# Kernel optimization log

Hardware: AMD Instinct MI355X
Metric: run time of the kernel (lower is better)

## Reference

```python
import jax, jax.numpy as jnp
import numpy as np

L = 5        # n_layers
H = 1024     # dim_in (hidden size)
DOUT = 1     # dim_out (input_size of LSTM)
T = 128      # curve_resolution
BS = 512


def setup_inputs() -> dict:
    key = jax.random.key(0)
    ks = jax.random.split(key, 8)
    s = 1.0 / np.sqrt(H)  # PyTorch LSTM default init scale U(-1/sqrt(H), 1/sqrt(H))
    x = jax.random.normal(ks[0], (BS, H), jnp.float32)
    W_ih0 = jax.random.normal(ks[1], (4 * H, DOUT), jnp.float32) * s
    W_ih_rest = jax.random.normal(ks[2], (L - 1, 4 * H, H), jnp.float32) * s
    W_hh = jax.random.normal(ks[3], (L, 4 * H, H), jnp.float32) * s
    b_ih = jax.random.normal(ks[4], (L, 4 * H), jnp.float32) * s
    b_hh = jax.random.normal(ks[5], (L, 4 * H), jnp.float32) * s
    W_ro = jax.random.normal(ks[6], (DOUT, H), jnp.float32) * s
    b_ro = jax.random.normal(ks[7], (DOUT,), jnp.float32) * s
    return {"x": x, "W_ih0": W_ih0, "W_ih_rest": W_ih_rest, "W_hh": W_hh,
            "b_ih": b_ih, "b_hh": b_hh, "W_ro": W_ro, "b_ro": b_ro}


def _cell(xin, h, c, W_ih, W_hh_l, b_ih_l, b_hh_l):
    # PyTorch gate order: i, f, g, o
    gates = xin @ W_ih.T + h @ W_hh_l.T + (b_ih_l + b_hh_l)
    i, f, g, o = jnp.split(gates, 4, axis=-1)
    c_new = jax.nn.sigmoid(f) * c + jax.nn.sigmoid(i) * jnp.tanh(g)
    h_new = jax.nn.sigmoid(o) * jnp.tanh(c_new)
    return h_new, c_new


def reference(x, W_ih0, W_ih_rest, W_hh, b_ih, b_hh, W_ro, b_ro):
    bs = x.shape[0]
    h0 = jnp.tile(x[None], (L, 1, 1))  # (L, bs, H) — graph emb as both h and c
    c0 = h0
    inp0 = jnp.zeros((bs, DOUT), x.dtype)

    def step(carry, _):
        h, c, inp = carry
        hs, cs = [], []
        xin = inp
        for l in range(L):
            W_ih_l = W_ih0 if l == 0 else W_ih_rest[l - 1]
            h_l, c_l = _cell(xin, h[l], c[l], W_ih_l, W_hh[l], b_ih[l], b_hh[l])
            hs.append(h_l)
            cs.append(c_l)
            xin = h_l
        out = xin @ W_ro.T + b_ro  # readout, fed back as next input
        return (jnp.stack(hs), jnp.stack(cs), out), out

    _, ys = jax.lax.scan(step, (h0, c0, inp0), None, length=T)
    return jnp.transpose(ys, (1, 0, 2))  # (bs, T, DOUT)
```

## Files before the change

kernel.cpp:

```cpp
#include <hip/hip_runtime.h>
#include <hip/hip_fp16.h>

#define LL 5
#define H 1024
#define G 4096
#define T 128
#define BS 512
#define BSH (BS * H)
#define BSG (BS * G)
#define GH  (G * H)

typedef _Float16 f16x8 __attribute__((ext_vector_type(8)));
typedef float f32x4 __attribute__((ext_vector_type(4)));

__device__ __forceinline__ float sigmoidf_(float x) { return 1.f / (1.f + __expf(-x)); }
__device__ __forceinline__ float tanhf_(float x) { return 2.f / (1.f + __expf(-2.f * x)) - 1.f; }

__device__ __forceinline__ void gll16(const void* g, void* l) {
  __builtin_amdgcn_global_load_lds(
      (const __attribute__((address_space(1))) void*)g,
      (__attribute__((address_space(3))) void*)l, 16, 0, 0);
}

#define VMW(N) asm volatile("s_waitcnt vmcnt(" #N ")" ::: "memory")
#define SBAR() asm volatile("s_barrier" ::: "memory")


__global__ void k_convert(const float* __restrict__ Whf, const float* __restrict__ Wxf,
                          __half* __restrict__ Whb, __half* __restrict__ Wxb) {
  const long long n1 = (long long)LL * GH / 4;
  const long long n2 = (long long)(LL - 1) * GH / 4;
  long long i = (long long)blockIdx.x * blockDim.x + threadIdx.x;
  long long stride = (long long)gridDim.x * blockDim.x;
  for (long long v = i; v < n1 + n2; v += stride) {
    const float4* src; __half* dst; long long idx;
    if (v < n1) { src = (const float4*)Whf; dst = Whb; idx = v; }
    else        { src = (const float4*)Wxf; dst = Wxb; idx = v - n1; }
    float4 f = src[idx];
    ushort4 u;
    u.x = __half_as_ushort(__float2half(f.x));
    u.y = __half_as_ushort(__float2half(f.y));
    u.z = __half_as_ushort(__float2half(f.z));
    u.w = __half_as_ushort(__float2half(f.w));
    ((ushort4*)dst)[idx] = u;
  }
}

__global__ void k_bias_y(const float* __restrict__ bih, const float* __restrict__ bhh,
                         float* __restrict__ bias, float* __restrict__ y0,
                         float* __restrict__ y1) {
  int i = blockIdx.x * blockDim.x + threadIdx.x;
  if (i < LL * G) bias[i] = bih[i] + bhh[i];
  if (i < BS) { y0[i] = 0.f; y1[i] = 0.f; }
}

__global__ void k_init(const float* __restrict__ x, __half* __restrict__ hbuf,
                       float* __restrict__ c) {
  int i = blockIdx.x * blockDim.x + threadIdx.x;
  if (i >= BS * H) return;
  float v = x[i];
  __half hb = __float2half(v);
  for (int l = 0; l < LL; l++) {
    hbuf[(long long)l * BSH + i] = hb;
    c[(long long)l * BSH + i] = v;
  }
}


#define SH_HALFS 24576

__device__ __forceinline__ void stage_tile(const __half* __restrict__ A,
                                           const __half* __restrict__ W,
                                           int m0, int jb, int kb,
                                           __half* aB, __half* bB,
                                           int wave, int lane) {
  const int i8 = lane >> 3;
  const int j8 = lane & 7;
  const int kch = j8 ^ i8;
#pragma unroll
  for (int s = 0; s < 2; s++) {
    int c = wave * 2 + s;
    int row = c * 8 + i8;
    gll16(A + (m0 + row) * H + kb + kch * 8, aB + c * 512);
  }
#pragma unroll
  for (int s = 0; s < 4; s++) {
    int c = wave * 4 + s;
    int row = c * 8 + i8;
    int grow = (row >> 5) * H + jb + (row & 31);
    gll16(W + grow * H + kb + kch * 8, bB + c * 512);
  }
}

__device__ __forceinline__ void compute_tile(const __half* aB, const __half* bB,
                                             int wave, int lane, f32x4 acc[2][4]) {
  const int quad = lane >> 4, col = lane & 15;
  const int wm = wave >> 1, wn = wave & 1;
  const int sw = col & 7;
#pragma unroll
  for (int ks = 0; ks < 2; ks++) {
    const int kc = ks * 4 + quad;
    const int kcs = kc ^ sw;
    f16x8 af[2], bf[4];
#pragma unroll
    for (int mt = 0; mt < 2; mt++) {
      int r = wm * 32 + mt * 16 + col;
      af[mt] = *(const f16x8*)(aB + ((r << 3) + kcs) * 8);
    }
#pragma unroll
    for (int nt = 0; nt < 4; nt++) {
      int n = nt * 32 + wn * 16 + col;
      bf[nt] = *(const f16x8*)(bB + ((n << 3) + kcs) * 8);
    }
#pragma unroll
    for (int mt = 0; mt < 2; mt++)
#pragma unroll
      for (int nt = 0; nt < 4; nt++)
        acc[mt][nt] = __builtin_amdgcn_mfma_f32_16x16x32_f16(af[mt], bf[nt], acc[mt][nt], 0, 0, 0);
  }
}

__device__ __forceinline__ void gemm_async(const __half* __restrict__ A,
                                           const __half* __restrict__ W,
                                           int m0, int jb, __half* sh, int t,
                                           f32x4 acc[2][4]) {
  const int wave = t >> 6, lane = t & 63;
  stage_tile(A, W, m0, jb, 0, sh, sh + 4096, wave, lane);
  for (int it = 0; it < 15; ++it) {
    const int cur = it & 1;
    stage_tile(A, W, m0, jb, (it + 1) * 64,
               sh + (cur ? 0 : 12288), sh + (cur ? 4096 : 16384), wave, lane);
    VMW(6);
    SBAR();
    compute_tile(sh + (cur ? 12288 : 0), sh + (cur ? 16384 : 4096), wave, lane, acc);
    SBAR();
  }
  VMW(0);
  SBAR();
  compute_tile(sh + 12288, sh + 16384, wave, lane, acc);
}

__device__ __forceinline__ void epilogue_store(f32x4 acc[2][4], __half* __restrict__ Ghout,
                                               const float* __restrict__ biasS,
                                               int m0, int jb, int t) {
  const int lane = t & 63, wave = t >> 6;
  const int quad = lane >> 4, col = lane & 15;
  const int wm = wave >> 1, wn = wave & 1;
  const int j = jb + wn * 16 + col;
  float bs[4];
#pragma unroll
  for (int nt = 0; nt < 4; nt++) bs[nt] = biasS[nt * H + j];
#pragma unroll
  for (int mt = 0; mt < 2; mt++)
#pragma unroll
    for (int nt = 0; nt < 4; nt++)
#pragma unroll
      for (int r = 0; r < 4; r++) {
        int b = m0 + wm * 32 + mt * 16 + quad * 4 + r;
        Ghout[b * G + nt * H + j] = __float2half(acc[mt][nt][r] + bs[nt]);
      }
}

__device__ __forceinline__ void epilogue_cell(f32x4 acc[2][4],
                                              const __half* __restrict__ Ghin,
                                              float* __restrict__ c, __half* __restrict__ hout,
                                              int m0, int jb, int t,
                                              const float* __restrict__ Wro,
                                              float* __restrict__ yAcc, float* red) {
  const int lane = t & 63, wave = t >> 6;
  const int quad = lane >> 4, col = lane & 15;
  const int wm = wave >> 1, wn = wave & 1;
  const int j = jb + wn * 16 + col;
  const float wj = Wro ? Wro[j] : 0.f;
#pragma unroll
  for (int mt = 0; mt < 2; mt++)
#pragma unroll
    for (int r = 0; r < 4; r++) {
      int row = wm * 32 + mt * 16 + quad * 4 + r;
      int b = m0 + row;
      float gi = acc[mt][0][r] + __half2float(Ghin[b * G + j]);
      float gf = acc[mt][1][r] + __half2float(Ghin[b * G + H + j]);
      float gg = acc[mt][2][r] + __half2float(Ghin[b * G + 2 * H + j]);
      float go = acc[mt][3][r] + __half2float(Ghin[b * G + 3 * H + j]);
      float cold = c[b * H + j];
      float cn = sigmoidf_(gf) * cold + sigmoidf_(gi) * tanhf_(gg);
      float hn = sigmoidf_(go) * tanhf_(cn);
      c[b * H + j] = cn;
      hout[b * H + j] = __float2half(hn);
      if (Wro) red[row * 33 + wn * 16 + col] = hn * wj;
    }
  if (Wro) {
    __syncthreads();
    if (t < 64) {
      float s = 0.f;
#pragma unroll
      for (int k = 0; k < 32; k++) s += red[t * 33 + k];
      atomicAdd(yAcc + m0 + t, s);
    }
  }
}


__global__ __launch_bounds__(256) void k_dual(
    const __half* __restrict__ A, const __half* __restrict__ Wc,
    const __half* __restrict__ Ws, const __half* __restrict__ Ghin,
    __half* __restrict__ Ghout, const float* __restrict__ biasS,
    float* __restrict__ c_, __half* __restrict__ hout,
    const float* __restrict__ Wro, float* __restrict__ yAcc,
    const __half* __restrict__ A2, const __half* __restrict__ Ws2,
    __half* __restrict__ Gh2, const float* __restrict__ bias2)
{
  __shared__ __half sh[SH_HALFS];
  const int t = threadIdx.x;
  const int jb = blockIdx.x * 32;
  const int m0 = blockIdx.y * 64;
  f32x4 acc[2][4];
#pragma unroll
  for (int a = 0; a < 2; a++)
#pragma unroll
    for (int b = 0; b < 4; b++) acc[a][b] = (f32x4){0.f, 0.f, 0.f, 0.f};
  if (blockIdx.z == 0) {
    gemm_async(A, Wc, m0, jb, sh, t, acc);
    epilogue_cell(acc, Ghin, c_, hout, m0, jb, t, Wro, yAcc, (float*)sh);
  } else if (blockIdx.z == 1) {
    gemm_async(A, Ws, m0, jb, sh, t, acc);
    epilogue_store(acc, Ghout, biasS, m0, jb, t);
  } else {
    gemm_async(A2, Ws2, m0, jb, sh, t, acc);
    epilogue_store(acc, Gh2, bias2, m0, jb, t);
  }
}

__global__ __launch_bounds__(256) void k_head(
    const __half* __restrict__ Gh0, const float* __restrict__ W0,
    const float* __restrict__ yA, float* __restrict__ yB,
    const float* __restrict__ bro, float* __restrict__ c0,
    __half* __restrict__ h0, float* __restrict__ out, int tPrev)
{
  int tid = blockIdx.x * 256 + threadIdx.x;
  for (int e4 = tid; e4 < BS * (H / 4); e4 += 32768) {
    int b = e4 >> 8;
    int j = (e4 & 255) << 2;
    float yv = yA[b];
    const __half2* p;
    p = (const __half2*)(Gh0 + b * G + j);
    float2 i01 = __half22float2(p[0]), i23 = __half22float2(p[1]);
    p = (const __half2*)(Gh0 + b * G + H + j);
    float2 f01 = __half22float2(p[0]), f23 = __half22float2(p[1]);
    p = (const __half2*)(Gh0 + b * G + 2 * H + j);
    float2 g01 = __half22float2(p[0]), g23 = __half22float2(p[1]);
    p = (const __half2*)(Gh0 + b * G + 3 * H + j);
    float2 o01 = __half22float2(p[0]), o23 = __half22float2(p[1]);
    float4 wi = *(const float4*)(W0 + j);
    float4 wf = *(const float4*)(W0 + H + j);
    float4 wg = *(const float4*)(W0 + 2 * H + j);
    float4 wo = *(const float4*)(W0 + 3 * H + j);
    float4 cc = *(const float4*)(c0 + b * H + j);
    float gi[4] = {i01.x + yv * wi.x, i01.y + yv * wi.y, i23.x + yv * wi.z, i23.y + yv * wi.w};
    float gf[4] = {f01.x + yv * wf.x, f01.y + yv * wf.y, f23.x + yv * wf.z, f23.y + yv * wf.w};
    float gg[4] = {g01.x + yv * wg.x, g01.y + yv * wg.y, g23.x + yv * wg.z, g23.y + yv * wg.w};
    float go[4] = {o01.x + yv * wo.x, o01.y + yv * wo.y, o23.x + yv * wo.z, o23.y + yv * wo.w};
    float cold[4] = {cc.x, cc.y, cc.z, cc.w};
    float cn[4], hn[4];
#pragma unroll
    for (int k = 0; k < 4; k++) {
      cn[k] = sigmoidf_(gf[k]) * cold[k] + sigmoidf_(gi[k]) * tanhf_(gg[k]);
      hn[k] = sigmoidf_(go[k]) * tanhf_(cn[k]);
    }
    *(float4*)(c0 + b * H + j) = (float4){cn[0], cn[1], cn[2], cn[3]};
    ushort4 hv;
    hv.x = __half_as_ushort(__float2half(hn[0]));
    hv.y = __half_as_ushort(__float2half(hn[1]));
    hv.z = __half_as_ushort(__float2half(hn[2]));
    hv.w = __half_as_ushort(__float2half(hn[3]));
    *(ushort4*)(h0 + b * H + j) = hv;
    if (j == 0) {
      if (tPrev >= 0) out[b * T + tPrev] = yv;
      yB[b] = bro[0];
    }
  }
}

__global__ __launch_bounds__(256) void k_init_gh(
    const __half* __restrict__ hb, const __half* __restrict__ WhbBase,
    __half* __restrict__ GhBase, const float* __restrict__ biasBase)
{
  __shared__ __half sh[SH_HALFS];
  const int t = threadIdx.x;
  const int jb = blockIdx.x * 32;
  const int m0 = blockIdx.y * 64;
  const int l = blockIdx.z;
  f32x4 acc[2][4];
#pragma unroll
  for (int a = 0; a < 2; a++)
#pragma unroll
    for (int b = 0; b < 4; b++) acc[a][b] = (f32x4){0.f, 0.f, 0.f, 0.f};
  gemm_async(hb + l * BSH, WhbBase + (long long)l * GH, m0, jb, sh, t, acc);
  epilogue_store(acc, GhBase + (long long)l * BSG, biasBase + l * G, m0, jb, t);
}

__global__ void k_tail(const float* __restrict__ yF, float* __restrict__ out) {
  int b = threadIdx.x + blockIdx.x * blockDim.x;
  if (b < BS) out[b * T + (T - 1)] = yF[b];
}

extern "C" void kernel_launch(void* const* d_in, const int* in_sizes, int n_in,
                              void* d_out, int out_size, void* d_ws, size_t ws_size,
                              hipStream_t stream) {
  const float* x    = (const float*)d_in[0];
  const float* Wih0 = (const float*)d_in[1];
  const float* Wxf  = (const float*)d_in[2];
  const float* Whf  = (const float*)d_in[3];
  const float* bih  = (const float*)d_in[4];
  const float* bhh  = (const float*)d_in[5];
  const float* Wro  = (const float*)d_in[6];
  const float* bro  = (const float*)d_in[7];
  float* out = (float*)d_out;

  char* ws = (char*)d_ws;
  __half* Whb  = (__half*)(ws);
  __half* Wxb  = (__half*)(ws + 41943040LL);
  __half* hbuf = (__half*)(ws + 75497472LL);
  float*  c    = (float*)(ws + 80740352LL);
  __half* Ghb  = (__half*)(ws + 91226112LL);
  float*  bias = (float*)(ws + 112197632LL);
  float*  y0   = (float*)(ws + 112279552LL);
  float*  y1   = (float*)(ws + 112281600LL);

  k_convert<<<2048, 256, 0, stream>>>(Whf, Wxf, Whb, Wxb);
  k_bias_y<<<80, 256, 0, stream>>>(bih, bhh, bias, y0, y1);
  k_init<<<2048, 256, 0, stream>>>(x, hbuf, c);
  k_init_gh<<<dim3(32, 8, 4), 256, 0, stream>>>(hbuf, Whb, Ghb, bias);

  for (int tst = 0; tst < T; ++tst) {
    float* yA = (tst & 1) ? y1 : y0;
    float* yB = (tst & 1) ? y0 : y1;
    k_head<<<128, 256, 0, stream>>>(Ghb, Wih0, yA, yB, bro, c, hbuf, out, tst - 1);
    for (int l = 1; l < LL; l++) {
      dim3 grid(32, 8, (l == 2) ? 3 : 2);
      k_dual<<<grid, 256, 0, stream>>>(
          hbuf + (l - 1) * BSH,
          Wxb + (long long)(l - 1) * GH,
          Whb + (long long)(l - 1) * GH,
          Ghb + l * BSG,
          Ghb + (l - 1) * BSG,
          bias + (l - 1) * G,
          c + l * BSH,
          hbuf + l * BSH,
          (l == 4) ? Wro : nullptr,
          (l == 4) ? yB : nullptr,
          hbuf + 4 * BSH,
          Whb + 4LL * GH,
          Ghb + 4 * BSG,
          bias + 4 * G);
    }
  }
  k_tail<<<1, 512, 0, stream>>>(y0, out);
}
```

Measured before the change: 9.300 ms.

## Fuse cell and state GEMMs sharing the A tile in one block

The two GEMMs that read the same hidden-state input (the input projection for the current layer and the recurrent projection for the previous layer) now run in a single block. That block stages the A tile once and accumulates two sets of accumulators from two B tiles. This halves the A-tile global loads and the number of blocks per launch. In exchange, LDS use per k_dual block rises to 80KB, register pressure grows with double accumulators, and fewer blocks are available to fill the CUs.

```diff
diff --git a/kernel.cpp b/kernel.cpp
--- a/kernel.cpp
+++ b/kernel.cpp
@@ -67,13 +67,10 @@
 }
 
 
-#define SH_HALFS 24576
-
-__device__ __forceinline__ void stage_tile(const __half* __restrict__ A,
-                                           const __half* __restrict__ W,
-                                           int m0, int jb, int kb,
-                                           __half* aB, __half* bB,
-                                           int wave, int lane) {
+#define SH_HALFS 40960
+
+__device__ __forceinline__ void stage_a(const __half* __restrict__ A,
+                                        int m0, int kb, __half* aB, int wave, int lane) {
   const int i8 = lane >> 3;
   const int j8 = lane & 7;
   const int kch = j8 ^ i8;
@@ -83,6 +80,13 @@
     int row = c * 8 + i8;
     gll16(A + (m0 + row) * H + kb + kch * 8, aB + c * 512);
   }
+}
+
+__device__ __forceinline__ void stage_b(const __half* __restrict__ W,
+                                        int jb, int kb, __half* bB, int wave, int lane) {
+  const int i8 = lane >> 3;
+  const int j8 = lane & 7;
+  const int kch = j8 ^ i8;
 #pragma unroll
   for (int s = 0; s < 4; s++) {
     int c = wave * 4 + s;
@@ -125,11 +129,12 @@
                                            int m0, int jb, __half* sh, int t,
                                            f32x4 acc[2][4]) {
   const int wave = t >> 6, lane = t & 63;
-  stage_tile(A, W, m0, jb, 0, sh, sh + 4096, wave, lane);
+  stage_a(A, m0, 0, sh, wave, lane);
+  stage_b(W, jb, 0, sh + 4096, wave, lane);
   for (int it = 0; it < 15; ++it) {
     const int cur = it & 1;
-    stage_tile(A, W, m0, jb, (it + 1) * 64,
-               sh + (cur ? 0 : 12288), sh + (cur ? 4096 : 16384), wave, lane);
+    stage_a(A, m0, (it + 1) * 64, sh + (cur ? 0 : 12288), wave, lane);
+    stage_b(W, jb, (it + 1) * 64, sh + (cur ? 4096 : 16384), wave, lane);
     VMW(6);
     SBAR();
     compute_tile(sh + (cur ? 12288 : 0), sh + (cur ? 16384 : 4096), wave, lane, acc);
@@ -138,6 +143,64 @@
   VMW(0);
   SBAR();
   compute_tile(sh + 12288, sh + 16384, wave, lane, acc);
+}
+
+__device__ __forceinline__ void compute_fused(const __half* aB, const __half* bcB,
+                                              const __half* bsB, int wave, int lane,
+                                              f32x4 accC[2][4], f32x4 accS[2][4]) {
+  const int quad = lane >> 4, col = lane & 15;
+  const int wm = wave >> 1, wn = wave & 1;
+  const int sw = col & 7;
+#pragma unroll
+  for (int ks = 0; ks < 2; ks++) {
+    const int kc = ks * 4 + quad;
+    const int kcs = kc ^ sw;
+    f16x8 af[2], bc[4], bs[4];
+#pragma unroll
+    for (int mt = 0; mt < 2; mt++) {
+      int r = wm * 32 + mt * 16 + col;
+      af[mt] = *(const f16x8*)(aB + ((r << 3) + kcs) * 8);
+    }
+#pragma unroll
+    for (int nt = 0; nt < 4; nt++) {
+      int n = nt * 32 + wn * 16 + col;
+      bc[nt] = *(const f16x8*)(bcB + ((n << 3) + kcs) * 8);
+      bs[nt] = *(const f16x8*)(bsB + ((n << 3) + kcs) * 8);
+    }
+#pragma unroll
+    for (int mt = 0; mt < 2; mt++)
+#pragma unroll
+      for (int nt = 0; nt < 4; nt++) {
+        accC[mt][nt] = __builtin_amdgcn_mfma_f32_16x16x32_f16(af[mt], bc[nt], accC[mt][nt], 0, 0, 0);
+        accS[mt][nt] = __builtin_amdgcn_mfma_f32_16x16x32_f16(af[mt], bs[nt], accS[mt][nt], 0, 0, 0);
+      }
+  }
+}
+
+__device__ __forceinline__ void gemm_fused(const __half* __restrict__ A,
+                                           const __half* __restrict__ Wc,
+                                           const __half* __restrict__ Ws,
+                                           int m0, int jb, __half* sh, int t,
+                                           f32x4 accC[2][4], f32x4 accS[2][4]) {
+  const int wave = t >> 6, lane = t & 63;
+  stage_a(A, m0, 0, sh, wave, lane);
+  stage_b(Wc, jb, 0, sh + 4096, wave, lane);
+  stage_b(Ws, jb, 0, sh + 12288, wave, lane);
+  for (int it = 0; it < 15; ++it) {
+    const int cur = it & 1;
+    const int nb = cur ? 0 : 20480;
+    stage_a(A, m0, (it + 1) * 64, sh + nb, wave, lane);
+    stage_b(Wc, jb, (it + 1) * 64, sh + nb + 4096, wave, lane);
+    stage_b(Ws, jb, (it + 1) * 64, sh + nb + 12288, wave, lane);
+    VMW(10);
+    SBAR();
+    const int cb = cur ? 20480 : 0;
+    compute_fused(sh + cb, sh + cb + 4096, sh + cb + 12288, wave, lane, accC, accS);
+    SBAR();
+  }
+  VMW(0);
+  SBAR();
+  compute_fused(sh + 20480, sh + 24576, sh + 32768, wave, lane, accC, accS);
 }
 
 __device__ __forceinline__ void epilogue_store(f32x4 acc[2][4], __half* __restrict__ Ghout,
@@ -214,18 +277,24 @@
   const int t = threadIdx.x;
   const int jb = blockIdx.x * 32;
   const int m0 = blockIdx.y * 64;
-  f32x4 acc[2][4];
-#pragma unroll
-  for (int a = 0; a < 2; a++)
-#pragma unroll
-    for (int b = 0; b < 4; b++) acc[a][b] = (f32x4){0.f, 0.f, 0.f, 0.f};
   if (blockIdx.z == 0) {
-    gemm_async(A, Wc, m0, jb, sh, t, acc);
-    epilogue_cell(acc, Ghin, c_, hout, m0, jb, t, Wro, yAcc, (float*)sh);
-  } else if (blockIdx.z == 1) {
-    gemm_async(A, Ws, m0, jb, sh, t, acc);
-    epilogue_store(acc, Ghout, biasS, m0, jb, t);
+    f32x4 accC[2][4], accS[2][4];
+#pragma unroll
+    for (int a = 0; a < 2; a++)
+#pragma unroll
+      for (int b = 0; b < 4; b++) {
+        accC[a][b] = (f32x4){0.f, 0.f, 0.f, 0.f};
+        accS[a][b] = (f32x4){0.f, 0.f, 0.f, 0.f};
+      }
+    gemm_fused(A, Wc, Ws, m0, jb, sh, t, accC, accS);
+    epilogue_store(accS, Ghout, biasS, m0, jb, t);
+    epilogue_cell(accC, Ghin, c_, hout, m0, jb, t, Wro, yAcc, (float*)sh);
   } else {
+    f32x4 acc[2][4];
+#pragma unroll
+    for (int a = 0; a < 2; a++)
+#pragma unroll
+      for (int b = 0; b < 4; b++) acc[a][b] = (f32x4){0.f, 0.f, 0.f, 0.f};
     gemm_async(A2, Ws2, m0, jb, sh, t, acc);
     epilogue_store(acc, Gh2, bias2, m0, jb, t);
   }
@@ -285,7 +354,7 @@
     const __half* __restrict__ hb, const __half* __restrict__ WhbBase,
     __half* __restrict__ GhBase, const float* __restrict__ biasBase)
 {
-  __shared__ __half sh[SH_HALFS];
+  __shared__ __half sh[24576];
   const int t = threadIdx.x;
   const int jb = blockIdx.x * 32;
   const int m0 = blockIdx.y * 64;
@@ -337,7 +406,7 @@
     float* yB = (tst & 1) ? y0 : y1;
     k_head<<<128, 256, 0, stream>>>(Ghb, Wih0, yA, yB, bro, c, hbuf, out, tst - 1);
     for (int l = 1; l < LL; l++) {
-      dim3 grid(32, 8, (l == 2) ? 3 : 2);
+      dim3 grid(32, 8, (l == 2) ? 2 : 1);
       k_dual<<<grid, 256, 0, stream>>>(
           hbuf + (l - 1) * BSH,
           Wxb + (long long)(l - 1) * GH,
```

New measurement: 11.79 ms. 26.8% more time.

## Load A operand fragments directly into registers instead of staging through LDS

Applied to the files above, without the earlier changes.

The GEMM's A-tile is no longer staged through shared memory. Each lane now issues global loads straight into MFMA-ready registers, double-buffered across iterations through two register sets, while only the weight tile still goes through LDS via async loads. The goal is to cut LDS traffic and the LDS footprint, which could allow higher occupancy. In exchange it uses more VGPRs, depends on a hand-counted vmcnt wait and inline asm, and may issue less coalesced global loads for A.

```diff
diff --git a/kernel.cpp b/kernel.cpp
--- a/kernel.cpp
+++ b/kernel.cpp
@@ -24,6 +24,12 @@
 
 #define VMW(N) asm volatile("s_waitcnt vmcnt(" #N ")" ::: "memory")
 #define SBAR() asm volatile("s_barrier" ::: "memory")
+
+__device__ __forceinline__ void load_a2(const __half* p, f16x8& a0, f16x8& a1) {
+  asm volatile("global_load_dwordx4 %0, %2, off\n\t"
+               "global_load_dwordx4 %1, %2, off offset:64"
+               : "=&v"(a0), "=&v"(a1) : "v"(p));
+}
 
 
 __global__ void k_convert(const float* __restrict__ Whf, const float* __restrict__ Wxf,
@@ -67,22 +73,13 @@
 }
 
 
-#define SH_HALFS 24576
-
-__device__ __forceinline__ void stage_tile(const __half* __restrict__ A,
-                                           const __half* __restrict__ W,
-                                           int m0, int jb, int kb,
-                                           __half* aB, __half* bB,
-                                           int wave, int lane) {
+#define SH_HALFS 16384
+
+__device__ __forceinline__ void stage_b(const __half* __restrict__ W,
+                                        int jb, int kb, __half* bB, int wave, int lane) {
   const int i8 = lane >> 3;
   const int j8 = lane & 7;
   const int kch = j8 ^ i8;
-#pragma unroll
-  for (int s = 0; s < 2; s++) {
-    int c = wave * 2 + s;
-    int row = c * 8 + i8;
-    gll16(A + (m0 + row) * H + kb + kch * 8, aB + c * 512);
-  }
 #pragma unroll
   for (int s = 0; s < 4; s++) {
     int c = wave * 4 + s;
@@ -92,31 +89,39 @@
   }
 }
 
-__device__ __forceinline__ void compute_tile(const __half* aB, const __half* bB,
-                                             int wave, int lane, f32x4 acc[2][4]) {
+__device__ __forceinline__ void compute_tile(const __half* bB, int wave, int lane,
+                                             f16x8 a00, f16x8 a01, f16x8 a10, f16x8 a11,
+                                             f32x4 acc[2][4]) {
   const int quad = lane >> 4, col = lane & 15;
-  const int wm = wave >> 1, wn = wave & 1;
+  const int wn = wave & 1;
   const int sw = col & 7;
-#pragma unroll
-  for (int ks = 0; ks < 2; ks++) {
-    const int kc = ks * 4 + quad;
-    const int kcs = kc ^ sw;
-    f16x8 af[2], bf[4];
-#pragma unroll
-    for (int mt = 0; mt < 2; mt++) {
-      int r = wm * 32 + mt * 16 + col;
-      af[mt] = *(const f16x8*)(aB + ((r << 3) + kcs) * 8);
-    }
+  {
+    const int kcs = quad ^ sw;
+    f16x8 bf[4];
 #pragma unroll
     for (int nt = 0; nt < 4; nt++) {
       int n = nt * 32 + wn * 16 + col;
       bf[nt] = *(const f16x8*)(bB + ((n << 3) + kcs) * 8);
     }
 #pragma unroll
-    for (int mt = 0; mt < 2; mt++)
-#pragma unroll
-      for (int nt = 0; nt < 4; nt++)
-        acc[mt][nt] = __builtin_amdgcn_mfma_f32_16x16x32_f16(af[mt], bf[nt], acc[mt][nt], 0, 0, 0);
+    for (int nt = 0; nt < 4; nt++) {
+      acc[0][nt] = __builtin_amdgcn_mfma_f32_16x16x32_f16(a00, bf[nt], acc[0][nt], 0, 0, 0);
+      acc[1][nt] = __builtin_amdgcn_mfma_f32_16x16x32_f16(a01, bf[nt], acc[1][nt], 0, 0, 0);
+    }
+  }
+  {
+    const int kcs = (4 + quad) ^ sw;
+    f16x8 bf[4];
+#pragma unroll
+    for (int nt = 0; nt < 4; nt++) {
+      int n = nt * 32 + wn * 16 + col;
+      bf[nt] = *(const f16x8*)(bB + ((n << 3) + kcs) * 8);
+    }
+#pragma unroll
+    for (int nt = 0; nt < 4; nt++) {
+      acc[0][nt] = __builtin_amdgcn_mfma_f32_16x16x32_f16(a10, bf[nt], acc[0][nt], 0, 0, 0);
+      acc[1][nt] = __builtin_amdgcn_mfma_f32_16x16x32_f16(a11, bf[nt], acc[1][nt], 0, 0, 0);
+    }
   }
 }
 
@@ -125,19 +130,39 @@
                                            int m0, int jb, __half* sh, int t,
                                            f32x4 acc[2][4]) {
   const int wave = t >> 6, lane = t & 63;
-  stage_tile(A, W, m0, jb, 0, sh, sh + 4096, wave, lane);
+  const int quad = lane >> 4, col = lane & 15;
+  const int wm = wave >> 1;
+  const __half* pA0 = A + (m0 + wm * 32 + col) * H + quad * 8;
+  const __half* pA1 = pA0 + 16 * H;
+  f16x8 a00, a01, a10, a11;
+  f16x8 b00, b01, b10, b11;
+  stage_b(W, jb, 0, sh, wave, lane);
+  load_a2(pA0, a00, a10);
+  load_a2(pA1, a01, a11);
+#pragma unroll
   for (int it = 0; it < 15; ++it) {
     const int cur = it & 1;
-    stage_tile(A, W, m0, jb, (it + 1) * 64,
-               sh + (cur ? 0 : 12288), sh + (cur ? 4096 : 16384), wave, lane);
-    VMW(6);
+    stage_b(W, jb, (it + 1) * 64, sh + (cur ? 0 : 8192), wave, lane);
+    if (it & 1) {
+      load_a2(pA0 + (it + 1) * 64, a00, a10);
+      load_a2(pA1 + (it + 1) * 64, a01, a11);
+    } else {
+      load_a2(pA0 + (it + 1) * 64, b00, b10);
+      load_a2(pA1 + (it + 1) * 64, b01, b11);
+    }
+    VMW(8);
     SBAR();
-    compute_tile(sh + (cur ? 12288 : 0), sh + (cur ? 16384 : 4096), wave, lane, acc);
+    __builtin_amdgcn_sched_barrier(0);
+    if (it & 1)
+      compute_tile(sh + 8192, wave, lane, b00, b01, b10, b11, acc);
+    else
+      compute_tile(sh, wave, lane, a00, a01, a10, a11, acc);
     SBAR();
   }
   VMW(0);
   SBAR();
-  compute_tile(sh + 12288, sh + 16384, wave, lane, acc);
+  __builtin_amdgcn_sched_barrier(0);
+  compute_tile(sh + 8192, wave, lane, b00, b01, b10, b11, acc);
 }
 
 __device__ __forceinline__ void epilogue_store(f32x4 acc[2][4], __half* __restrict__ Ghout,
```

Measured after the change: 13.69 ms. 1.47x slower.
